# Performance work log

Hardware: AMD Instinct MI355X
Metric: run time of the kernel (lower is better)

## Reference

```python
import jax, jax.numpy as jnp
import numpy as np

E = 1024
FF = 4096
EPS = 1e-5


def _linear(x, W, b):
    # x: [B,S,in], W: [in,out], b: [out]
    return jnp.einsum('bsi,io->bso', x, W) + b


def _layernorm(x, g, b):
    mu = jnp.mean(x, axis=-1, keepdims=True)
    var = jnp.mean(jnp.square(x - mu), axis=-1, keepdims=True)
    return (x - mu) * jax.lax.rsqrt(var + EPS) * g + b


def setup_inputs() -> dict:
    key = jax.random.key(0)
    ks = jax.random.split(key, 8)
    s = 0.02
    inp = {
        'src': jax.random.normal(ks[0], (4, 2048, E), dtype=jnp.float32),
        'Wq': jax.random.normal(ks[1], (E, E), dtype=jnp.float32) * s,
        'bq': jnp.zeros((E,), jnp.float32),
        'Wk': jax.random.normal(ks[2], (E, E), dtype=jnp.float32) * s,
        'bk': jnp.zeros((E,), jnp.float32),
        'Wv': jax.random.normal(ks[3], (E, E), dtype=jnp.float32) * s,
        'bv': jnp.zeros((E,), jnp.float32),
        'Wo': jax.random.normal(ks[4], (E, E), dtype=jnp.float32) * s,
        'bo': jnp.zeros((E,), jnp.float32),
        'W1': jax.random.normal(ks[5], (E, FF), dtype=jnp.float32) * s,
        'b1': jnp.zeros((FF,), jnp.float32),
        'W2': jax.random.normal(ks[6], (FF, E), dtype=jnp.float32) * s,
        'b2': jnp.zeros((E,), jnp.float32),
        'g1': jnp.ones((E,), jnp.float32),
        'be1': jnp.zeros((E,), jnp.float32),
        'g2': jnp.ones((E,), jnp.float32),
        'be2': jnp.zeros((E,), jnp.float32),
    }
    return inp


def reference(src, Wq, bq, Wk, bk, Wv, bv, Wo, bo, W1, b1, W2, b2, g1, be1, g2, be2):
    Q = _linear(src, Wq, bq)
    K = _linear(src, Wk, bk)
    V = _linear(src, Wv, bv)
    # Single-head attention, NO 1/sqrt(d) scaling (faithful to source)
    scores = jnp.einsum('bqe,bke->bqk', Q, K)  # [B,S,S]
    weights = jax.nn.softmax(scores, axis=-1)
    attn = jnp.einsum('bqk,bke->bqe', weights, V)
    attn = _linear(attn, Wo, bo)
    x = _layernorm(src + attn, g1, be1)
    ff = _linear(x, W1, b1)
    ff = jax.nn.relu(ff)
    ff = _linear(ff, W2, b2)
    return _layernorm(x + ff, g2, be2)
```

## Files before the change

kernel.cpp:

```cpp
#include <hip/hip_runtime.h>
#include <hip/hip_bf16.h>


using u16 = unsigned short;
typedef __attribute__((ext_vector_type(8))) _Float16 half8;
typedef __attribute__((ext_vector_type(4))) float f32x4;

#define BATCH 4
#define SEQ   2048
#define EMB   1024
#define FFD   4096

#define SWZ(r) ((((r) >> 1) & 3) << 4)

__device__ __forceinline__ u16 f2h(float f) {
    union { _Float16 h; u16 u; } x;
    x.h = (_Float16)f;
    return x.u;
}
__device__ __forceinline__ float h2f(u16 u) {
    union { u16 u; _Float16 h; } x;
    x.u = u;
    return (float)x.h;
}

typedef const __attribute__((address_space(1))) void* gas_ptr;
typedef __attribute__((address_space(3))) void* las_ptr;

__device__ __forceinline__ void load_lds16(const void* g, void* l) {
    __builtin_amdgcn_global_load_lds((gas_ptr)g, (las_ptr)l, 16, 0, 0);
}

template <typename OutT, bool RELU, bool BIAS>
__global__ __launch_bounds__(512, 2) void gemm_8p(
    const u16* __restrict__ A, const u16* __restrict__ Bt,
    OutT* __restrict__ C, const float* __restrict__ bias,
    int N, int K, int lda, int ldb, int ldc, long sA, long sB, long sC)
{
    constexpr int BUF = 65536;
    __shared__ __attribute__((aligned(16))) char lds[2 * BUF];

    A  += (long)blockIdx.z * sA;
    Bt += (long)blockIdx.z * sB;
    C  += (long)blockIdx.z * sC;

    const int tid  = threadIdx.x;
    const int lane = tid & 63;
    const int wv   = tid >> 6;
    const int wm   = wv >> 2;
    const int wn   = wv & 3;
    const long row0 = (long)blockIdx.x * 256;
    const long col0 = (long)blockIdx.y * 256;

    long aS[2], bS[2]; int dD[2];
#pragma unroll
    for (int i = 0; i < 2; ++i) {
        const int d16 = i * 512 + tid;
        const int lrow = d16 >> 3;
        const int sl   = d16 & 7;
        const long cswz = (long)((sl ^ (lrow & 7)) << 3);
        aS[i] = (row0 + lrow) * (long)lda + cswz;
        bS[i] = (col0 + lrow) * (long)ldb + cswz;
        dD[i] = d16 * 16;
    }
    const long aHop = 128 * (long)lda;
    const long bHop = 128 * (long)ldb;

    const int klb = (lane >> 4) << 4;
    const int swz = (lane & 7) << 4;
    const int aRB = (wm * 128 + (lane & 15)) * 128 + (klb ^ swz);
    const int bRB = 32768 + (wn * 64 + (lane & 15)) * 128 + (klb ^ swz);

    f32x4 acc[8][4] = {};
    half8 a[8], b[4];
    const int G = K >> 6;

#define SGA(BUFB, H, KT)                                                      \
    { _Pragma("unroll") for (int i_ = 0; i_ < 2; ++i_)                        \
          load_lds16(A + aS[i_] + (H) * aHop + (long)(KT) * 64,               \
                     lds + (BUFB) + (H) * 16384 + dD[i_]); }
#define SGB(BUFB, H, KT)                                                      \
    { _Pragma("unroll") for (int i_ = 0; i_ < 2; ++i_)                        \
          load_lds16(Bt + bS[i_] + (H) * bHop + (long)(KT) * 64,              \
                     lds + (BUFB) + 32768 + (H) * 16384 + dD[i_]); }
#define NOP8 ((void)0)
#define VM8 asm volatile("s_waitcnt vmcnt(8)" ::: "memory")
#define VM6 asm volatile("s_waitcnt vmcnt(6)" ::: "memory")
#define VM2 asm volatile("s_waitcnt vmcnt(2)" ::: "memory")
#define VMZ asm volatile("s_waitcnt vmcnt(0)" ::: "memory")

#define PH8(BUFB, QM, QN, RDA, RDB, STG, VM)                                  \
    {                                                                         \
        if (RDA) {                                                            \
            _Pragma("unroll") for (int m_ = 0; m_ < 4; ++m_)                  \
            _Pragma("unroll") for (int k_ = 0; k_ < 2; ++k_)                  \
                a[m_ * 2 + k_] = *(const half8*)(lds + (BUFB) +               \
                    ((aRB + (QM) * 8192 + m_ * 2048) ^ (k_ << 6)));           \
        }                                                                     \
        if (RDB) {                                                            \
            _Pragma("unroll") for (int n_ = 0; n_ < 2; ++n_)                  \
            _Pragma("unroll") for (int k_ = 0; k_ < 2; ++k_)                  \
                b[n_ * 2 + k_] = *(const half8*)(lds + (BUFB) +               \
                    ((bRB + (QN) * 4096 + n_ * 2048) ^ (k_ << 6)));           \
        }                                                                     \
        STG; VM;                                                              \
        __builtin_amdgcn_s_barrier();                                         \
        asm volatile("s_waitcnt lgkmcnt(0)" ::: "memory");                    \
        __builtin_amdgcn_sched_barrier(0);                                    \
        __builtin_amdgcn_s_setprio(1);                                        \
        _Pragma("unroll") for (int k_ = 0; k_ < 2; ++k_)                      \
        _Pragma("unroll") for (int m_ = 0; m_ < 4; ++m_)                      \
        _Pragma("unroll") for (int n_ = 0; n_ < 2; ++n_)                      \
            acc[(QM) * 4 + m_][(QN) * 2 + n_] =                               \
                __builtin_amdgcn_mfma_f32_16x16x32_f16(                       \
                    a[m_ * 2 + k_], b[n_ * 2 + k_],                           \
                    acc[(QM) * 4 + m_][(QN) * 2 + n_], 0, 0, 0);              \
        __builtin_amdgcn_s_setprio(0);                                        \
        __builtin_amdgcn_s_barrier();                                         \
    }

    SGA(0, 0, 0); SGB(0, 1, 0); SGB(0, 0, 0); SGA(0, 1, 0);
    SGA(BUF, 0, 1); SGB(BUF, 1, 1);
    VM6;
    __builtin_amdgcn_s_barrier();

    for (int t = 0; t < G - 2; ++t) {
        const int cb = (t & 1) * BUF, ob = cb ^ BUF;
        PH8(cb, 0, 0, 1, 1, SGB(ob, 0, t + 1), NOP8)
        PH8(cb, 0, 1, 0, 1, SGA(ob, 1, t + 1), VM8)
        PH8(cb, 1, 1, 1, 0, SGA(cb, 0, t + 2), NOP8)
        PH8(cb, 1, 0, 0, 1, SGB(cb, 1, t + 2), VM6)
    }
    {
        const int cb = ((G - 2) & 1) * BUF, ob = cb ^ BUF;
        PH8(cb, 0, 0, 1, 1, SGB(ob, 0, G - 1), NOP8)
        PH8(cb, 0, 1, 0, 1, SGA(ob, 1, G - 1), VM8)
        PH8(cb, 1, 1, 1, 0, NOP8, NOP8)
        PH8(cb, 1, 0, 0, 1, NOP8, VM2)
    }
    {
        const int cb = ((G - 1) & 1) * BUF;
        PH8(cb, 0, 0, 1, 1, NOP8, NOP8)
        PH8(cb, 0, 1, 0, 1, NOP8, VMZ)
        PH8(cb, 1, 1, 1, 0, NOP8, NOP8)
        PH8(cb, 1, 0, 0, 1, NOP8, NOP8)
    }
#undef PH8
#undef SGA
#undef SGB
#undef NOP8
#undef VM8
#undef VM6
#undef VM2
#undef VMZ

    long cofs[4]; float bb[4];
#pragma unroll
    for (int n = 0; n < 4; ++n) {
        cofs[n] = col0 + wn * 64 + (n >> 1) * 32 + (n & 1) * 16 + (lane & 15);
        bb[n] = BIAS ? bias[cofs[n]] : 0.0f;
    }
#pragma unroll
    for (int m = 0; m < 8; ++m) {
#pragma unroll
        for (int r = 0; r < 4; ++r) {
            const long row = row0 + wm * 128 + (m >> 2) * 64 + (m & 3) * 16 +
                             ((lane >> 4) << 2) + r;
            OutT* Crow = C + row * (long)ldc;
#pragma unroll
            for (int n = 0; n < 4; ++n) {
                float v = acc[m][n][r] + bb[n];
                if (RELU) v = fmaxf(v, 0.0f);
                if constexpr (sizeof(OutT) == 2)
                    Crow[cofs[n]] = f2h(v);
                else
                    Crow[cofs[n]] = v;
            }
        }
    }
}

template <int BM, typename OutT, bool RELU, bool BIAS>
__global__ __launch_bounds__(512, 2) void gemm_dp(
    const u16* __restrict__ A, const u16* __restrict__ Bt,
    OutT* __restrict__ C, const float* __restrict__ bias,
    int N, int K, int lda, int ldb, int ldc, long sA, long sB, long sC)
{
    constexpr int MF = BM / 32;
    constexpr int AL = BM / 128;
    constexpr int SLAB_A = BM * 32;
    constexpr int SLAB_B = 256 * 32;

    __shared__ u16 ldsA[4 * SLAB_A];
    __shared__ u16 ldsB[4 * SLAB_B];

    A  += (long)blockIdx.z * sA;
    Bt += (long)blockIdx.z * sB;
    C  += (long)blockIdx.z * sC;

    const int tid  = threadIdx.x;
    const int lane = tid & 63;
    const int wv   = tid >> 6;
    const int wm   = wv >> 2;
    const int wn   = wv & 3;
    const long row0 = (long)blockIdx.x * BM;
    const long col0 = (long)blockIdx.y * 256;

    long aoff[AL]; int adst[AL];
#pragma unroll
    for (int i = 0; i < AL; ++i) {
        const int d16 = i * 512 + tid;
        const int row = d16 >> 2;
        const int colb = ((d16 & 3) << 4) ^ SWZ(row);
        aoff[i] = (row0 + row) * (long)lda + (colb >> 1);
        adst[i] = d16 * 16;
    }
    long boff[2]; int bdst[2];
#pragma unroll
    for (int i = 0; i < 2; ++i) {
        const int d16 = i * 512 + tid;
        const int row = d16 >> 2;
        const int colb = ((d16 & 3) << 4) ^ SWZ(row);
        boff[i] = (col0 + row) * (long)ldb + (colb >> 1);
        bdst[i] = d16 * 16;
    }

    int aro[MF], bro[4];
    const int klane = (lane >> 4) << 4;
#pragma unroll
    for (int m = 0; m < MF; ++m) {
        const int row = wm * (BM / 2) + m * 16 + (lane & 15);
        aro[m] = row * 64 + (klane ^ SWZ(row));
    }
#pragma unroll
    for (int n = 0; n < 4; ++n) {
        const int row = wn * 64 + n * 16 + (lane & 15);
        bro[n] = row * 64 + (klane ^ SWZ(row));
    }

    f32x4 acc[MF][4] = {};
    const int G = K >> 5;

    auto stage = [&](int g) {
        const int slot = g & 3;
        const long k0 = (long)g << 5;
#pragma unroll
        for (int i = 0; i < AL; ++i)
            load_lds16(A + aoff[i] + k0, (char*)ldsA + slot * (SLAB_A * 2) + adst[i]);
#pragma unroll
        for (int i = 0; i < 2; ++i)
            load_lds16(Bt + boff[i] + k0, (char*)ldsB + slot * (SLAB_B * 2) + bdst[i]);
    };

#define VMS asm volatile("s_waitcnt vmcnt(6)" ::: "memory")
#define VMT asm volatile("s_waitcnt vmcnt(3)" ::: "memory")
#define VM0 asm volatile("s_waitcnt vmcnt(0)" ::: "memory")
#define VMNONE ((void)0)

#define GBODY(g, VMASM, DOSTAGE)                                              \
    {                                                                         \
        const int slot_ = (g) & 3;                                            \
        const char* abase_ = (const char*)ldsA + slot_ * (SLAB_A * 2);        \
        const char* bbase_ = (const char*)ldsB + slot_ * (SLAB_B * 2);        \
        half8 a_[MF], b_[4];                                                  \
        _Pragma("unroll") for (int m = 0; m < MF; ++m)                        \
            a_[m] = *(const half8*)(abase_ + aro[m]);                         \
        _Pragma("unroll") for (int n = 0; n < 4; ++n)                         \
            b_[n] = *(const half8*)(bbase_ + bro[n]);                         \
        if (DOSTAGE) stage((g) + 3);                                          \
        VMASM;                                                                \
        __builtin_amdgcn_s_setprio(1);                                        \
        _Pragma("unroll") for (int m = 0; m < MF; ++m)                        \
            _Pragma("unroll") for (int n = 0; n < 4; ++n)                     \
                acc[m][n] = __builtin_amdgcn_mfma_f32_16x16x32_f16(           \
                    a_[m], b_[n], acc[m][n], 0, 0, 0);                        \
        __builtin_amdgcn_s_setprio(0);                                        \
        __builtin_amdgcn_s_barrier();                                         \
        __builtin_amdgcn_sched_barrier(0);                                    \
    }

    stage(0); stage(1); stage(2);
    VMS;
    __builtin_amdgcn_s_barrier();
    __builtin_amdgcn_sched_barrier(0);

    for (int g = 0; g < G - 3; ++g) GBODY(g, VMS, true)
    GBODY(G - 3, VMT, false)
    GBODY(G - 2, VM0, false)
    GBODY(G - 1, VMNONE, false)
#undef GBODY
#undef VMS
#undef VMT
#undef VM0
#undef VMNONE

#pragma unroll
    for (int n = 0; n < 4; ++n) {
        const long col = col0 + wn * 64 + n * 16 + (lane & 15);
        const float bv_ = BIAS ? bias[col] : 0.0f;
#pragma unroll
        for (int m = 0; m < MF; ++m) {
            const long row = row0 + wm * (BM / 2) + m * 16 + ((lane >> 4) << 2);
#pragma unroll
            for (int r = 0; r < 4; ++r) {
                float v = acc[m][n][r] + bv_;
                if (RELU) v = fmaxf(v, 0.0f);
                if constexpr (sizeof(OutT) == 2)
                    C[(row + r) * (long)ldc + col] = f2h(v);
                else
                    C[(row + r) * (long)ldc + col] = v;
            }
        }
    }
}

__global__ __launch_bounds__(256) void tc4(
    const float* __restrict__ s0, const float* __restrict__ s1,
    const float* __restrict__ s2, const float* __restrict__ s3,
    u16* __restrict__ dqkv, u16* __restrict__ dwo)
{
    __shared__ float t[32][33];
    const int z = blockIdx.z;
    const float* in = (z == 0) ? s0 : (z == 1) ? s1 : (z == 2) ? s2 : s3;
    u16* out = (z < 3) ? (dqkv + (long)z * EMB * EMB) : dwo;
    const int bc = blockIdx.x * 32, br = blockIdx.y * 32;
    const int lx = threadIdx.x & 31, ly = threadIdx.x >> 5;
#pragma unroll
    for (int i = 0; i < 32; i += 8)
        t[ly + i][lx] = in[(long)(br + ly + i) * EMB + bc + lx];
    __syncthreads();
#pragma unroll
    for (int i = 0; i < 32; i += 8)
        out[(long)(bc + ly + i) * EMB + br + lx] = f2h(t[lx][ly + i]);
}

__global__ __launch_bounds__(256) void transpose_cast(
    const float* __restrict__ in, u16* __restrict__ out, int R, int C)
{
    __shared__ float t[32][33];
    const int bc = blockIdx.x * 32, br = blockIdx.y * 32;
    const int lx = threadIdx.x & 31, ly = threadIdx.x >> 5;
#pragma unroll
    for (int i = 0; i < 32; i += 8)
        t[ly + i][lx] = in[(long)(br + ly + i) * C + bc + lx];
    __syncthreads();
#pragma unroll
    for (int i = 0; i < 32; i += 8)
        out[(long)(bc + ly + i) * R + br + lx] = f2h(t[lx][ly + i]);
}

__global__ __launch_bounds__(256) void transpose_h(
    const u16* __restrict__ in, u16* __restrict__ out,
    int ldin, int ldout, long sIn, long sOut)
{
    __shared__ u16 t[32][33];
    in  += (long)blockIdx.z * sIn;
    out += (long)blockIdx.z * sOut;
    const int bc = blockIdx.x * 32, br = blockIdx.y * 32;
    const int lx = threadIdx.x & 31, ly = threadIdx.x >> 5;
#pragma unroll
    for (int i = 0; i < 32; i += 8)
        t[ly + i][lx] = in[(long)(br + ly + i) * ldin + bc + lx];
    __syncthreads();
#pragma unroll
    for (int i = 0; i < 32; i += 8)
        out[(long)(bc + ly + i) * ldout + br + lx] = t[lx][ly + i];
}

__global__ __launch_bounds__(256) void cast_h(
    const float* __restrict__ in, u16* __restrict__ out)
{
    const long i = ((long)blockIdx.x * 256 + threadIdx.x) * 8;
    const float4 a = ((const float4*)(in + i))[0];
    const float4 b = ((const float4*)(in + i))[1];
    union { u16 u[8]; uint4 v; } pk;
    pk.u[0] = f2h(a.x); pk.u[1] = f2h(a.y); pk.u[2] = f2h(a.z); pk.u[3] = f2h(a.w);
    pk.u[4] = f2h(b.x); pk.u[5] = f2h(b.y); pk.u[6] = f2h(b.z); pk.u[7] = f2h(b.w);
    *(uint4*)(out + i) = pk.v;
}

__global__ __launch_bounds__(256) void concat_bias(
    const float* __restrict__ bq, const float* __restrict__ bk,
    const float* __restrict__ bv, float* __restrict__ o)
{
    const int i = blockIdx.x * 256 + threadIdx.x;
    o[i] = i < 1024 ? bq[i] : (i < 2048 ? bk[i - 1024] : bv[i - 2048]);
}

__global__ __launch_bounds__(256) void softmax_kernel(
    const u16* __restrict__ S, u16* __restrict__ P)
{
    const long row = blockIdx.x;
    const int tid = threadIdx.x;

    union { uint4 v; u16 u[8]; } in;
    in.v = ((const uint4*)(S + row * SEQ))[tid];
    float f[8];
#pragma unroll
    for (int j = 0; j < 8; ++j) f[j] = h2f(in.u[j]);

    float m = fmaxf(fmaxf(fmaxf(f[0], f[1]), fmaxf(f[2], f[3])),
                    fmaxf(fmaxf(f[4], f[5]), fmaxf(f[6], f[7])));
#pragma unroll
    for (int off = 32; off; off >>= 1) m = fmaxf(m, __shfl_xor(m, off));

    __shared__ float rm[4], rs[4];
    if ((tid & 63) == 0) rm[tid >> 6] = m;
    __syncthreads();
    m = fmaxf(fmaxf(rm[0], rm[1]), fmaxf(rm[2], rm[3]));

    float e[8], s = 0.0f;
#pragma unroll
    for (int j = 0; j < 8; ++j) { e[j] = expf(f[j] - m); s += e[j]; }
#pragma unroll
    for (int off = 32; off; off >>= 1) s += __shfl_xor(s, off);
    if ((tid & 63) == 0) rs[tid >> 6] = s;
    __syncthreads();
    s = (rs[0] + rs[1]) + (rs[2] + rs[3]);

    const float inv = 1.0f / s;
    union { u16 u[8]; uint4 v; } pk;
#pragma unroll
    for (int j = 0; j < 8; ++j) pk.u[j] = f2h(e[j] * inv);
    *(uint4*)(P + row * SEQ + tid * 8) = pk.v;
}

template <bool A16, bool OUT16>
__global__ __launch_bounds__(256) void ln_kernel(
    const void* __restrict__ Ain, const u16* __restrict__ Bin,
    const float* __restrict__ g, const float* __restrict__ be,
    void* __restrict__ Out)
{
    const long row = blockIdx.x;
    const int tid = threadIdx.x;

    float a0, a1, a2, a3;
    if constexpr (A16) {
        union { uint2 v; u16 u[4]; } av;
        av.v = ((const uint2*)((const u16*)Ain + row * EMB))[tid];
        a0 = h2f(av.u[0]); a1 = h2f(av.u[1]); a2 = h2f(av.u[2]); a3 = h2f(av.u[3]);
    } else {
        const float4 av = ((const float4*)((const float*)Ain + row * EMB))[tid];
        a0 = av.x; a1 = av.y; a2 = av.z; a3 = av.w;
    }
    union { uint2 v; u16 u[4]; } bv16;
    bv16.v = ((const uint2*)(Bin + row * EMB))[tid];
    const float h0 = a0 + h2f(bv16.u[0]);
    const float h1 = a1 + h2f(bv16.u[1]);
    const float h2 = a2 + h2f(bv16.u[2]);
    const float h3 = a3 + h2f(bv16.u[3]);

    float s = (h0 + h1) + (h2 + h3);
    float q = (h0 * h0 + h1 * h1) + (h2 * h2 + h3 * h3);
#pragma unroll
    for (int off = 32; off; off >>= 1) {
        s += __shfl_xor(s, off);
        q += __shfl_xor(q, off);
    }
    __shared__ float rsm[4], rqm[4];
    if ((tid & 63) == 0) { rsm[tid >> 6] = s; rqm[tid >> 6] = q; }
    __syncthreads();
    s = (rsm[0] + rsm[1]) + (rsm[2] + rsm[3]);
    q = (rqm[0] + rqm[1]) + (rqm[2] + rqm[3]);

    const float mu  = s * (1.0f / EMB);
    const float var = q * (1.0f / EMB) - mu * mu;
    const float rstd = rsqrtf(var + 1e-5f);

    const float4 gv = ((const float4*)g)[tid];
    const float4 bv = ((const float4*)be)[tid];
    const float y0 = (h0 - mu) * rstd * gv.x + bv.x;
    const float y1 = (h1 - mu) * rstd * gv.y + bv.y;
    const float y2 = (h2 - mu) * rstd * gv.z + bv.z;
    const float y3 = (h3 - mu) * rstd * gv.w + bv.w;

    if constexpr (OUT16) {
        union { u16 u[4]; uint2 v; } pk;
        pk.u[0] = f2h(y0); pk.u[1] = f2h(y1);
        pk.u[2] = f2h(y2); pk.u[3] = f2h(y3);
        ((uint2*)((u16*)Out + row * EMB))[tid] = pk.v;
    } else {
        ((float4*)((float*)Out + row * EMB))[tid] = make_float4(y0, y1, y2, y3);
    }
}

extern "C" void kernel_launch(void* const* d_in, const int* in_sizes, int n_in,
                              void* d_out, int out_size, void* d_ws, size_t ws_size,
                              hipStream_t stream)
{
    const float* src = (const float*)d_in[0];
    const float* Wq  = (const float*)d_in[1];
    const float* bq  = (const float*)d_in[2];
    const float* Wk  = (const float*)d_in[3];
    const float* bk  = (const float*)d_in[4];
    const float* Wv  = (const float*)d_in[5];
    const float* bv  = (const float*)d_in[6];
    const float* Wo  = (const float*)d_in[7];
    const float* bo  = (const float*)d_in[8];
    const float* W1  = (const float*)d_in[9];
    const float* b1  = (const float*)d_in[10];
    const float* W2  = (const float*)d_in[11];
    const float* b2  = (const float*)d_in[12];
    const float* g1  = (const float*)d_in[13];
    const float* be1 = (const float*)d_in[14];
    const float* g2  = (const float*)d_in[15];
    const float* be2 = (const float*)d_in[16];
    float* out = (float*)d_out;

    char* ws = (char*)d_ws;
    const size_t MB = 1ull << 20;
    u16*   WqkvT   = (u16*)  (ws + 0 * MB);
    u16*   WoT     = (u16*)  (ws + 6 * MB);
    u16*   W1T     = (u16*)  (ws + 8 * MB);
    u16*   W2T     = (u16*)  (ws + 16 * MB);
    float* bqkv    = (float*)(ws + 24 * MB);
    u16*   Xh      = (u16*)  (ws + 25 * MB);
    u16*   QKVh    = (u16*)  (ws + 41 * MB);
    u16*   Vt      = (u16*)  (ws + 89 * MB);
    u16*   scoresh = (u16*)  (ws + 105 * MB);
    u16*   P       = (u16*)  (ws + 137 * MB);
    u16*   attn    = (u16*)  (ws + 105 * MB);
    u16*   attnp   = (u16*)  (ws + 121 * MB);
    u16*   x       = (u16*)  (ws + 137 * MB);
    u16*   ff1     = (u16*)  (ws + 41 * MB);
    u16*   ff2     = (u16*)  (ws + 105 * MB);

    const int M = BATCH * SEQ;
    const long SS = (long)SEQ * SEQ;

    tc4<<<dim3(32, 32, 4), 256, 0, stream>>>(Wq, Wk, Wv, Wo, WqkvT, WoT);
    transpose_cast<<<dim3(128, 32, 1), 256, 0, stream>>>(W1, W1T, EMB, FFD);
    transpose_cast<<<dim3(32, 128, 1), 256, 0, stream>>>(W2, W2T, FFD, EMB);
    concat_bias<<<dim3(12), 256, 0, stream>>>(bq, bk, bv, bqkv);

    cast_h<<<dim3((M * EMB) / (256 * 8)), 256, 0, stream>>>(src, Xh);

    gemm_8p<u16, false, true><<<dim3(32, 12, 1), 512, 0, stream>>>(
        Xh, WqkvT, QKVh, bqkv, 3072, 1024, 1024, 1024, 3072, 0, 0, 0);

    transpose_h<<<dim3(32, 64, BATCH), 256, 0, stream>>>(
        QKVh + 2048, Vt, 3072, SEQ, (long)SEQ * 3072, (long)EMB * SEQ);

    gemm_8p<u16, false, false><<<dim3(8, 8, BATCH), 512, 0, stream>>>(
        QKVh, QKVh + 1024, scoresh, nullptr, SEQ, EMB, 3072, 3072, SEQ,
        (long)SEQ * 3072, (long)SEQ * 3072, SS);

    softmax_kernel<<<dim3(M), 256, 0, stream>>>(scoresh, P);

    gemm_dp<128, u16, false, false><<<dim3(16, 4, BATCH), 512, 0, stream>>>(
        P, Vt, attn, nullptr, EMB, SEQ, SEQ, SEQ, EMB,
        SS, (long)EMB * SEQ, (long)SEQ * EMB);

    gemm_dp<128, u16, false, true><<<dim3(64, 4, 1), 512, 0, stream>>>(
        attn, WoT, attnp, bo, EMB, EMB, EMB, EMB, EMB, 0, 0, 0);

    ln_kernel<false, true><<<dim3(M), 256, 0, stream>>>(
        src, attnp, g1, be1, x);

    gemm_8p<u16, true, true><<<dim3(32, 16, 1), 512, 0, stream>>>(
        x, W1T, ff1, b1, FFD, EMB, EMB, EMB, FFD, 0, 0, 0);

    gemm_dp<128, u16, false, true><<<dim3(64, 4, 1), 512, 0, stream>>>(
        ff1, W2T, ff2, b2, EMB, FFD, FFD, FFD, EMB, 0, 0, 0);

    ln_kernel<true, false><<<dim3(M), 256, 0, stream>>>(
        x, ff2, g2, be2, out);
}
```

Measured before the change: 392.9 us.

## Remap GEMM LDS quadrants and prefetch next A fragment across phases

Reorganizes the 256x256 GEMM tile so each LDS quadrant holds interleaved row groups matching the per-wave fragment layout. The kernel now keeps double register fragments (a0/a1, b0/b1) and reads the next tile's first A fragment during the last phase, with a uniform vmcnt(6) wait per phase. The aim is finer-grained global-to-LDS staging and more overlap of LDS reads with MFMA. It raises register pressure, and the changed wait counts and cross-buffer read ordering risk subtle hazards.

```diff
diff --git a/kernel.cpp b/kernel.cpp
--- a/kernel.cpp
+++ b/kernel.cpp
@@ -59,100 +59,99 @@
         const int lrow = d16 >> 3;
         const int sl   = d16 & 7;
         const long cswz = (long)((sl ^ (lrow & 7)) << 3);
-        aS[i] = (row0 + lrow) * (long)lda + cswz;
-        bS[i] = (col0 + lrow) * (long)ldb + cswz;
+        aS[i] = (row0 + (lrow >> 6) * 128 + (lrow & 63)) * (long)lda + cswz;
+        bS[i] = (col0 + (lrow >> 5) * 64 + (lrow & 31)) * (long)ldb + cswz;
         dD[i] = d16 * 16;
     }
-    const long aHop = 128 * (long)lda;
-    const long bHop = 128 * (long)ldb;
 
     const int klb = (lane >> 4) << 4;
     const int swz = (lane & 7) << 4;
-    const int aRB = (wm * 128 + (lane & 15)) * 128 + (klb ^ swz);
-    const int bRB = 32768 + (wn * 64 + (lane & 15)) * 128 + (klb ^ swz);
+    const int aRB = (wm * 64 + (lane & 15)) * 128 + (klb ^ swz);
+    const int bRB = 32768 + (wn * 32 + (lane & 15)) * 128 + (klb ^ swz);
 
     f32x4 acc[8][4] = {};
-    half8 a[8], b[4];
+    half8 a0[8], a1[8], b0[4], b1[4];
     const int G = K >> 6;
 
-#define SGA(BUFB, H, KT)                                                      \
+#define SGA(BUFB, Q, KT)                                                      \
     { _Pragma("unroll") for (int i_ = 0; i_ < 2; ++i_)                        \
-          load_lds16(A + aS[i_] + (H) * aHop + (long)(KT) * 64,               \
-                     lds + (BUFB) + (H) * 16384 + dD[i_]); }
-#define SGB(BUFB, H, KT)                                                      \
+          load_lds16(A + aS[i_] + (long)(Q) * 64 * lda + (long)(KT) * 64,     \
+                     lds + (BUFB) + (Q) * 16384 + dD[i_]); }
+#define SGB(BUFB, Q, KT)                                                      \
     { _Pragma("unroll") for (int i_ = 0; i_ < 2; ++i_)                        \
-          load_lds16(Bt + bS[i_] + (H) * bHop + (long)(KT) * 64,              \
-                     lds + (BUFB) + 32768 + (H) * 16384 + dD[i_]); }
-#define NOP8 ((void)0)
-#define VM8 asm volatile("s_waitcnt vmcnt(8)" ::: "memory")
+          load_lds16(Bt + bS[i_] + (long)(Q) * 32 * ldb + (long)(KT) * 64,    \
+                     lds + (BUFB) + 32768 + (Q) * 16384 + dD[i_]); }
+#define RDA(dst, BUFB, Q)                                                     \
+    { _Pragma("unroll") for (int m_ = 0; m_ < 4; ++m_)                        \
+      _Pragma("unroll") for (int k_ = 0; k_ < 2; ++k_)                        \
+          dst[m_ * 2 + k_] = *(const half8*)(lds + (BUFB) + (Q) * 16384 +     \
+              ((aRB + m_ * 2048) ^ (k_ << 6))); }
+#define RDB(dst, BUFB, Q)                                                     \
+    { _Pragma("unroll") for (int n_ = 0; n_ < 2; ++n_)                        \
+      _Pragma("unroll") for (int k_ = 0; k_ < 2; ++k_)                        \
+          dst[n_ * 2 + k_] = *(const half8*)(lds + (BUFB) + (Q) * 16384 +     \
+              ((bRB + n_ * 2048) ^ (k_ << 6))); }
+#define MM(AX, BX, QM, QN)                                                    \
+    { __builtin_amdgcn_s_setprio(1);                                          \
+      _Pragma("unroll") for (int k_ = 0; k_ < 2; ++k_)                        \
+      _Pragma("unroll") for (int m_ = 0; m_ < 4; ++m_)                        \
+      _Pragma("unroll") for (int n_ = 0; n_ < 2; ++n_)                        \
+          acc[(QM) * 4 + m_][(QN) * 2 + n_] =                                 \
+              __builtin_amdgcn_mfma_f32_16x16x32_f16(                         \
+                  AX[m_ * 2 + k_], BX[n_ * 2 + k_],                           \
+                  acc[(QM) * 4 + m_][(QN) * 2 + n_], 0, 0, 0);                \
+      __builtin_amdgcn_s_setprio(0); }
+#define NOPS ((void)0)
 #define VM6 asm volatile("s_waitcnt vmcnt(6)" ::: "memory")
+#define VM4 asm volatile("s_waitcnt vmcnt(4)" ::: "memory")
 #define VM2 asm volatile("s_waitcnt vmcnt(2)" ::: "memory")
-#define VMZ asm volatile("s_waitcnt vmcnt(0)" ::: "memory")
-
-#define PH8(BUFB, QM, QN, RDA, RDB, STG, VM)                                  \
-    {                                                                         \
-        if (RDA) {                                                            \
-            _Pragma("unroll") for (int m_ = 0; m_ < 4; ++m_)                  \
-            _Pragma("unroll") for (int k_ = 0; k_ < 2; ++k_)                  \
-                a[m_ * 2 + k_] = *(const half8*)(lds + (BUFB) +               \
-                    ((aRB + (QM) * 8192 + m_ * 2048) ^ (k_ << 6)));           \
-        }                                                                     \
-        if (RDB) {                                                            \
-            _Pragma("unroll") for (int n_ = 0; n_ < 2; ++n_)                  \
-            _Pragma("unroll") for (int k_ = 0; k_ < 2; ++k_)                  \
-                b[n_ * 2 + k_] = *(const half8*)(lds + (BUFB) +               \
-                    ((bRB + (QN) * 4096 + n_ * 2048) ^ (k_ << 6)));           \
-        }                                                                     \
-        STG; VM;                                                              \
-        __builtin_amdgcn_s_barrier();                                         \
-        asm volatile("s_waitcnt lgkmcnt(0)" ::: "memory");                    \
-        __builtin_amdgcn_sched_barrier(0);                                    \
-        __builtin_amdgcn_s_setprio(1);                                        \
-        _Pragma("unroll") for (int k_ = 0; k_ < 2; ++k_)                      \
-        _Pragma("unroll") for (int m_ = 0; m_ < 4; ++m_)                      \
-        _Pragma("unroll") for (int n_ = 0; n_ < 2; ++n_)                      \
-            acc[(QM) * 4 + m_][(QN) * 2 + n_] =                               \
-                __builtin_amdgcn_mfma_f32_16x16x32_f16(                       \
-                    a[m_ * 2 + k_], b[n_ * 2 + k_],                           \
-                    acc[(QM) * 4 + m_][(QN) * 2 + n_], 0, 0, 0);              \
-        __builtin_amdgcn_s_setprio(0);                                        \
-        __builtin_amdgcn_s_barrier();                                         \
-    }
-
-    SGA(0, 0, 0); SGB(0, 1, 0); SGB(0, 0, 0); SGA(0, 1, 0);
-    SGA(BUF, 0, 1); SGB(BUF, 1, 1);
+#define VM0 asm volatile("s_waitcnt vmcnt(0)" ::: "memory")
+#define PH(RD, STG, VM, MMA)                                                  \
+    { RD; STG; VM;                                                            \
+      __builtin_amdgcn_s_barrier();                                           \
+      asm volatile("s_waitcnt lgkmcnt(0)" ::: "memory");                      \
+      __builtin_amdgcn_sched_barrier(0);                                      \
+      MMA;                                                                    \
+      __builtin_amdgcn_s_barrier(); }
+
+    SGA(0, 0, 0); SGB(0, 0, 0); SGB(0, 1, 0); SGA(0, 1, 0);
+    SGA(BUF, 0, 1);
     VM6;
     __builtin_amdgcn_s_barrier();
+    RDA(a0, 0, 0);
 
     for (int t = 0; t < G - 2; ++t) {
         const int cb = (t & 1) * BUF, ob = cb ^ BUF;
-        PH8(cb, 0, 0, 1, 1, SGB(ob, 0, t + 1), NOP8)
-        PH8(cb, 0, 1, 0, 1, SGA(ob, 1, t + 1), VM8)
-        PH8(cb, 1, 1, 1, 0, SGA(cb, 0, t + 2), NOP8)
-        PH8(cb, 1, 0, 0, 1, SGB(cb, 1, t + 2), VM6)
+        PH(RDB(b0, cb, 0), SGB(ob, 0, t + 1), VM6, MM(a0, b0, 0, 0))
+        PH(RDB(b1, cb, 1), SGB(ob, 1, t + 1), VM6, MM(a0, b1, 0, 1))
+        PH(RDA(a1, cb, 1), SGA(ob, 1, t + 1), VM6, MM(a1, b1, 1, 1))
+        PH(RDA(a0, ob, 0), SGA(cb, 0, t + 2), VM6, MM(a1, b0, 1, 0))
     }
     {
         const int cb = ((G - 2) & 1) * BUF, ob = cb ^ BUF;
-        PH8(cb, 0, 0, 1, 1, SGB(ob, 0, G - 1), NOP8)
-        PH8(cb, 0, 1, 0, 1, SGA(ob, 1, G - 1), VM8)
-        PH8(cb, 1, 1, 1, 0, NOP8, NOP8)
-        PH8(cb, 1, 0, 0, 1, NOP8, VM2)
+        PH(RDB(b0, cb, 0), SGB(ob, 0, G - 1), VM6, MM(a0, b0, 0, 0))
+        PH(RDB(b1, cb, 1), SGB(ob, 1, G - 1), VM6, MM(a0, b1, 0, 1))
+        PH(RDA(a1, cb, 1), SGA(ob, 1, G - 1), VM6, MM(a1, b1, 1, 1))
+        PH(RDA(a0, ob, 0), NOPS,              VM4, MM(a1, b0, 1, 0))
     }
     {
         const int cb = ((G - 1) & 1) * BUF;
-        PH8(cb, 0, 0, 1, 1, NOP8, NOP8)
-        PH8(cb, 0, 1, 0, 1, NOP8, VMZ)
-        PH8(cb, 1, 1, 1, 0, NOP8, NOP8)
-        PH8(cb, 1, 0, 0, 1, NOP8, NOP8)
-    }
-#undef PH8
+        PH(RDB(b0, cb, 0), NOPS, VM2, MM(a0, b0, 0, 0))
+        PH(RDB(b1, cb, 1), NOPS, VM0, MM(a0, b1, 0, 1))
+        PH(RDA(a1, cb, 1), NOPS, NOPS, MM(a1, b1, 1, 1))
+        PH(NOPS,           NOPS, NOPS, MM(a1, b0, 1, 0))
+    }
+#undef PH
 #undef SGA
 #undef SGB
-#undef NOP8
-#undef VM8
+#undef RDA
+#undef RDB
+#undef MM
+#undef NOPS
 #undef VM6
+#undef VM4
 #undef VM2
-#undef VMZ
+#undef VM0
 
     long cofs[4]; float bb[4];
 #pragma unroll
```

Result: no change. 393.4 us (+0.1%).

## Compute V transposed directly via swapped-operand GEMM, dropping the transpose pass

Applied to the files above, without the earlier changes.

The V projection is split out of the fused QKV GEMM. It is computed as Wv^T·X^T with a new row-bias mode, so V^T is written directly, and the separate transpose_h kernel over V is removed. The first layernorm now reads the half-precision Xh residual instead of fp32 src, which cuts bytes read but adds fp16 rounding to the residual. The cost is an extra GEMM launch with a smaller N per GEMM, which may lower utilisation.

```diff
diff --git a/kernel.cpp b/kernel.cpp
--- a/kernel.cpp
+++ b/kernel.cpp
@@ -180,7 +180,7 @@
     }
 }
 
-template <int BM, typename OutT, bool RELU, bool BIAS>
+template <int BM, typename OutT, bool RELU, int BMODE>
 __global__ __launch_bounds__(512, 2) void gemm_dp(
     const u16* __restrict__ A, const u16* __restrict__ Bt,
     OutT* __restrict__ C, const float* __restrict__ bias,
@@ -297,13 +297,14 @@
 #pragma unroll
     for (int n = 0; n < 4; ++n) {
         const long col = col0 + wn * 64 + n * 16 + (lane & 15);
-        const float bv_ = BIAS ? bias[col] : 0.0f;
+        const float bc_ = (BMODE == 1) ? bias[col] : 0.0f;
 #pragma unroll
         for (int m = 0; m < MF; ++m) {
             const long row = row0 + wm * (BM / 2) + m * 16 + ((lane >> 4) << 2);
 #pragma unroll
             for (int r = 0; r < 4; ++r) {
-                float v = acc[m][n][r] + bv_;
+                float v = acc[m][n][r] + bc_;
+                if (BMODE == 2) v += bias[row + r];
                 if (RELU) v = fmaxf(v, 0.0f);
                 if constexpr (sizeof(OutT) == 2)
                     C[(row + r) * (long)ldc + col] = f2h(v);
@@ -317,12 +318,12 @@
 __global__ __launch_bounds__(256) void tc4(
     const float* __restrict__ s0, const float* __restrict__ s1,
     const float* __restrict__ s2, const float* __restrict__ s3,
-    u16* __restrict__ dqkv, u16* __restrict__ dwo)
+    u16* __restrict__ dqk, u16* __restrict__ dwv, u16* __restrict__ dwo)
 {
     __shared__ float t[32][33];
     const int z = blockIdx.z;
     const float* in = (z == 0) ? s0 : (z == 1) ? s1 : (z == 2) ? s2 : s3;
-    u16* out = (z < 3) ? (dqkv + (long)z * EMB * EMB) : dwo;
+    u16* out = (z < 2) ? (dqk + (long)z * EMB * EMB) : (z == 2 ? dwv : dwo);
     const int bc = blockIdx.x * 32, br = blockIdx.y * 32;
     const int lx = threadIdx.x & 31, ly = threadIdx.x >> 5;
 #pragma unroll
@@ -347,24 +348,6 @@
 #pragma unroll
     for (int i = 0; i < 32; i += 8)
         out[(long)(bc + ly + i) * R + br + lx] = f2h(t[lx][ly + i]);
-}
-
-__global__ __launch_bounds__(256) void transpose_h(
-    const u16* __restrict__ in, u16* __restrict__ out,
-    int ldin, int ldout, long sIn, long sOut)
-{
-    __shared__ u16 t[32][33];
-    in  += (long)blockIdx.z * sIn;
-    out += (long)blockIdx.z * sOut;
-    const int bc = blockIdx.x * 32, br = blockIdx.y * 32;
-    const int lx = threadIdx.x & 31, ly = threadIdx.x >> 5;
-#pragma unroll
-    for (int i = 0; i < 32; i += 8)
-        t[ly + i][lx] = in[(long)(br + ly + i) * ldin + bc + lx];
-    __syncthreads();
-#pragma unroll
-    for (int i = 0; i < 32; i += 8)
-        out[(long)(bc + ly + i) * ldout + br + lx] = t[lx][ly + i];
 }
 
 __global__ __launch_bounds__(256) void cast_h(
@@ -381,10 +364,10 @@
 
 __global__ __launch_bounds__(256) void concat_bias(
     const float* __restrict__ bq, const float* __restrict__ bk,
-    const float* __restrict__ bv, float* __restrict__ o)
+    float* __restrict__ o)
 {
     const int i = blockIdx.x * 256 + threadIdx.x;
-    o[i] = i < 1024 ? bq[i] : (i < 2048 ? bk[i - 1024] : bv[i - 2048]);
+    o[i] = i < 1024 ? bq[i] : bk[i - 1024];
 }
 
 __global__ __launch_bounds__(256) void softmax_kernel(
@@ -509,58 +492,60 @@
 
     char* ws = (char*)d_ws;
     const size_t MB = 1ull << 20;
-    u16*   WqkvT   = (u16*)  (ws + 0 * MB);
+    u16*   WqkT    = (u16*)  (ws + 0 * MB);
+    u16*   WvT     = (u16*)  (ws + 4 * MB);
     u16*   WoT     = (u16*)  (ws + 6 * MB);
     u16*   W1T     = (u16*)  (ws + 8 * MB);
     u16*   W2T     = (u16*)  (ws + 16 * MB);
-    float* bqkv    = (float*)(ws + 24 * MB);
+    float* bqk     = (float*)(ws + 24 * MB);
     u16*   Xh      = (u16*)  (ws + 25 * MB);
-    u16*   QKVh    = (u16*)  (ws + 41 * MB);
-    u16*   Vt      = (u16*)  (ws + 89 * MB);
-    u16*   scoresh = (u16*)  (ws + 105 * MB);
-    u16*   P       = (u16*)  (ws + 137 * MB);
-    u16*   attn    = (u16*)  (ws + 105 * MB);
-    u16*   attnp   = (u16*)  (ws + 121 * MB);
-    u16*   x       = (u16*)  (ws + 137 * MB);
+    u16*   QKh     = (u16*)  (ws + 41 * MB);
+    u16*   Vt      = (u16*)  (ws + 73 * MB);
+    u16*   scoresh = (u16*)  (ws + 89 * MB);
+    u16*   P       = (u16*)  (ws + 121 * MB);
+    u16*   attn    = (u16*)  (ws + 89 * MB);
+    u16*   attnp   = (u16*)  (ws + 105 * MB);
+    u16*   x       = (u16*)  (ws + 121 * MB);
     u16*   ff1     = (u16*)  (ws + 41 * MB);
     u16*   ff2     = (u16*)  (ws + 105 * MB);
 
     const int M = BATCH * SEQ;
     const long SS = (long)SEQ * SEQ;
 
-    tc4<<<dim3(32, 32, 4), 256, 0, stream>>>(Wq, Wk, Wv, Wo, WqkvT, WoT);
+    tc4<<<dim3(32, 32, 4), 256, 0, stream>>>(Wq, Wk, Wv, Wo, WqkT, WvT, WoT);
     transpose_cast<<<dim3(128, 32, 1), 256, 0, stream>>>(W1, W1T, EMB, FFD);
     transpose_cast<<<dim3(32, 128, 1), 256, 0, stream>>>(W2, W2T, FFD, EMB);
-    concat_bias<<<dim3(12), 256, 0, stream>>>(bq, bk, bv, bqkv);
+    concat_bias<<<dim3(8), 256, 0, stream>>>(bq, bk, bqk);
 
     cast_h<<<dim3((M * EMB) / (256 * 8)), 256, 0, stream>>>(src, Xh);
 
-    gemm_8p<u16, false, true><<<dim3(32, 12, 1), 512, 0, stream>>>(
-        Xh, WqkvT, QKVh, bqkv, 3072, 1024, 1024, 1024, 3072, 0, 0, 0);
-
-    transpose_h<<<dim3(32, 64, BATCH), 256, 0, stream>>>(
-        QKVh + 2048, Vt, 3072, SEQ, (long)SEQ * 3072, (long)EMB * SEQ);
+    gemm_8p<u16, false, true><<<dim3(32, 8, 1), 512, 0, stream>>>(
+        Xh, WqkT, QKh, bqk, 2048, 1024, 1024, 1024, 2048, 0, 0, 0);
+
+    gemm_dp<128, u16, false, 2><<<dim3(8, 8, BATCH), 512, 0, stream>>>(
+        WvT, Xh, Vt, bv, SEQ, 1024, 1024, 1024, SEQ,
+        0, (long)SEQ * EMB, (long)EMB * SEQ);
 
     gemm_8p<u16, false, false><<<dim3(8, 8, BATCH), 512, 0, stream>>>(
-        QKVh, QKVh + 1024, scoresh, nullptr, SEQ, EMB, 3072, 3072, SEQ,
-        (long)SEQ * 3072, (long)SEQ * 3072, SS);
+        QKh, QKh + 1024, scoresh, nullptr, SEQ, 1024, 2048, 2048, SEQ,
+        (long)SEQ * 2048, (long)SEQ * 2048, SS);
 
     softmax_kernel<<<dim3(M), 256, 0, stream>>>(scoresh, P);
 
-    gemm_dp<128, u16, false, false><<<dim3(16, 4, BATCH), 512, 0, stream>>>(
+    gemm_dp<128, u16, false, 0><<<dim3(16, 4, BATCH), 512, 0, stream>>>(
         P, Vt, attn, nullptr, EMB, SEQ, SEQ, SEQ, EMB,
         SS, (long)EMB * SEQ, (long)SEQ * EMB);
 
-    gemm_dp<128, u16, false, true><<<dim3(64, 4, 1), 512, 0, stream>>>(
+    gemm_dp<128, u16, false, 1><<<dim3(64, 4, 1), 512, 0, stream>>>(
         attn, WoT, attnp, bo, EMB, EMB, EMB, EMB, EMB, 0, 0, 0);
 
-    ln_kernel<false, true><<<dim3(M), 256, 0, stream>>>(
-        src, attnp, g1, be1, x);
+    ln_kernel<true, true><<<dim3(M), 256, 0, stream>>>(
+        Xh, attnp, g1, be1, x);
 
     gemm_8p<u16, true, true><<<dim3(32, 16, 1), 512, 0, stream>>>(
         x, W1T, ff1, b1, FFD, EMB, EMB, EMB, FFD, 0, 0, 0);
 
-    gemm_dp<128, u16, false, true><<<dim3(64, 4, 1), 512, 0, stream>>>(
+    gemm_dp<128, u16, false, 1><<<dim3(64, 4, 1), 512, 0, stream>>>(
         ff1, W2T, ff2, b2, EMB, FFD, FFD, FFD, EMB, 0, 0, 0);
 
     ln_kernel<true, false><<<dim3(M), 256, 0, stream>>>(
```

Result: faster. 385.0 us (-2.0%).
